# Performance work log

Hardware: AMD Instinct MI355X
Metric: run time of the kernel (lower is better)

The kernel has to match this reference:

```python
import jax, jax.numpy as jnp
import numpy as np

B, D_IN, D_FEAT, N_EX, N_LAB = 4096, 512, 512, 20000, 100
P_FACTOR = 3.0
EPS = 1e-12  # torch F.normalize eps


def setup_inputs() -> dict:
    key = jax.random.key(0)
    k1, k2, k3, k4 = jax.random.split(key, 4)
    features = jax.random.normal(k1, (B, D_IN), dtype=jnp.float32)
    g_weight = jax.random.normal(k2, (D_FEAT, D_IN), dtype=jnp.float32) * (1.0 / np.sqrt(D_IN))
    ex_features = jax.random.normal(k3, (N_EX, D_IN), dtype=jnp.float32)
    ex_classes = jax.random.uniform(k4, (N_EX, N_LAB), dtype=jnp.float32)
    class_reps = jnp.eye(N_LAB, dtype=jnp.float32)  # one_hot(arange(num_labels)) since class_dim is None
    return {"features": features, "g_weight": g_weight, "ex_features": ex_features,
            "ex_classes": ex_classes, "class_reps": class_reps}


def _l2_normalize(x):
    n = jnp.linalg.norm(x, axis=-1, keepdims=True)
    return x / jnp.maximum(n, EPS)


def _l1_normalize(x):
    n = jnp.sum(jnp.abs(x), axis=-1, keepdims=True)
    return x / jnp.maximum(n, EPS)


def reference(features, g_weight, ex_features, ex_classes, class_reps):
    # g projection (bias-free linear)
    f = features @ g_weight.T          # [B, D_FEAT]
    e = ex_features @ g_weight.T       # [N_EX, D_FEAT]
    # exemplar class representations
    ex_class_reps = _l1_normalize(ex_classes) @ class_reps  # [N_EX, N_LAB]
    # cosine similarity
    s = _l2_normalize(f) @ _l2_normalize(e).T  # [B, N_EX]
    # power-sign activation then L1 row-normalize
    a = jnp.sign(s) * jnp.abs(s) ** P_FACTOR
    a = _l1_normalize(a)
    echo = a @ ex_class_reps           # [B, N_LAB]
    return echo
```

## Files before the change

kernel.cpp:

```cpp
#include <hip/hip_runtime.h>

#define B_ROWS 4096
#define D      512
#define N_EX   20000
#define EXP2   20096
#define MPROJ  24192
#define N_LAB  100
#define LABP2  128
#define NT2    157
#define SPLITS 16

typedef __attribute__((ext_vector_type(8)))  short short8v;
typedef __attribute__((ext_vector_type(16))) float f32x16;
typedef __attribute__((ext_vector_type(2)))  int   int2v;
typedef unsigned short u16;

__device__ __forceinline__ u16 f2bf(float x) {
    unsigned u = __builtin_bit_cast(unsigned, x);
    u = u + 0x7FFFu + ((u >> 16) & 1u);
    return (u16)(u >> 16);
}
__device__ __forceinline__ float bf2f(u16 h) {
    unsigned u = ((unsigned)h) << 16;
    return __builtin_bit_cast(float, u);
}

__device__ __forceinline__ void gload16(const void* g, void* l) {
    __builtin_amdgcn_global_load_lds((const __attribute__((address_space(1))) void*)g,
                                     (__attribute__((address_space(3))) void*)l, 16, 0, 0);
}

__device__ __forceinline__ unsigned pk_bf16(float a, float b) {
    unsigned r;
    asm("v_cvt_pk_bf16_f32 %0, %1, %2" : "=v"(r) : "v"(a), "v"(b));
    return r;
}

__device__ __forceinline__ void swap_halves(unsigned &a, unsigned &b) {
#if __has_builtin(__builtin_amdgcn_permlane32_swap)
    int2v r = __builtin_amdgcn_permlane32_swap((int)a, (int)b, false, false);
    a = (unsigned)r[0]; b = (unsigned)r[1];
#else
    unsigned sa = (unsigned)__shfl_xor((int)a, 32, 64);
    unsigned sb = (unsigned)__shfl_xor((int)b, 32, 64);
    if (threadIdx.x & 32) a = sb; else b = sa;
#endif
}

#define MFMA32(a, b, c) __builtin_amdgcn_mfma_f32_32x32x16_bf16((a), (b), (c), 0, 0, 0)

__global__ __launch_bounds__(256)
void split3_k(const float* __restrict__ f, const float* __restrict__ ex,
              const float* __restrict__ gw, u16* __restrict__ xall,
              u16* __restrict__ wh) {
    int i8 = blockIdx.x * 256 + threadIdx.x;
    int row = i8 >> 6;
    int e = (i8 & 63) * 8;
    const float* src = nullptr;
    u16* dst;
    if (row < B_ROWS) {
        src = &f[(size_t)row * D + e];
        dst = &xall[(size_t)row * D + e];
    } else if (row < B_ROWS + EXP2) {
        int er = row - B_ROWS;
        if (er < N_EX) src = &ex[(size_t)er * D + e];
        dst = &xall[(size_t)row * D + e];
    } else if (row < B_ROWS + EXP2 + D) {
        int wr = row - B_ROWS - EXP2;
        src = &gw[(size_t)wr * D + e];
        dst = &wh[(size_t)wr * D + e];
    } else return;
    short8v h = {0,0,0,0,0,0,0,0};
    if (src) {
        float4 a = *(const float4*)src, b = *(const float4*)(src + 4);
        float v[8] = {a.x,a.y,a.z,a.w,b.x,b.y,b.z,b.w};
        #pragma unroll
        for (int j = 0; j < 8; ++j) h[j] = (short)f2bf(v[j]);
    }
    *(short8v*)dst = h;
}

__global__ __launch_bounds__(512, 4)
void gemm128_k(const u16* __restrict__ A, const u16* __restrict__ B,
               u16* __restrict__ C) {
    __shared__ u16 BUF[2][128][128];
    const int tid = threadIdx.x;
    const int l = tid & 63, w = tid >> 6;
    const int wa = w >> 2, wb = w & 3;
    const int l31 = l & 31, l5 = l >> 5;
    const int m0 = blockIdx.x * 128, n0 = blockIdx.y * 128;
    const int qrow_in = l >> 4;
    const int gs = l & 15;

    f32x16 sacc[2] = {};

    auto STAGE = [&](int nx, int kc_) {
        const int kofs = kc_ * 64;
        #pragma unroll
        for (int i = 0; i < 4; ++i) {
            const int q = w * 4 + i;
            const int r = q * 4 + qrow_in;
            const int g = gs ^ (r & 15);
            const u16* src = (g < 8)
                ? &A[(size_t)(m0 + r) * D + kofs + g * 8]
                : &B[(size_t)(n0 + r) * D + kofs + (g - 8) * 8];
            gload16(src, (u16*)&BUF[nx][0][0] + q * 512);
        }
    };

    STAGE(0, 0);
    __syncthreads();
    int cur = 0;
    for (int kc = 0; kc < 8; ++kc) {
        if (kc < 7) STAGE(cur ^ 1, kc + 1);
        const u16* base = &BUF[cur][0][0];
        #pragma unroll
        for (int ks = 0; ks < 4; ++ks) {
            const int gk = ks * 2 + l5;
            short8v aX[2], bW;
            #pragma unroll
            for (int ei = 0; ei < 2; ++ei) {
                int r = wa * 64 + ei * 32 + l31;
                aX[ei] = *(const short8v*)(base + r * 128 + (gk ^ (r & 15)) * 8);
            }
            {
                int r = wb * 32 + l31;
                bW = *(const short8v*)(base + r * 128 + ((gk | 8) ^ (r & 15)) * 8);
            }
            sacc[0] = MFMA32(aX[0], bW, sacc[0]);
            sacc[1] = MFMA32(aX[1], bW, sacc[1]);
        }
        __syncthreads();
        cur ^= 1;
    }
    #pragma unroll
    for (int ei = 0; ei < 2; ++ei)
        #pragma unroll
        for (int r = 0; r < 16; ++r) {
            int row = m0 + wa * 64 + ei * 32 + (r & 3) + 8 * (r >> 2) + 4 * l5;
            int col = n0 + wb * 32 + l31;
            C[(size_t)row * D + col] = f2bf(sacc[ei][r]);
        }
}

__global__ __launch_bounds__(256)
void l2norm_k(u16* __restrict__ hi, int nrows) {
    const int row = blockIdx.x * 4 + (threadIdx.x >> 6);
    const int ln = threadIdx.x & 63;
    if (row >= nrows) return;
    const size_t base = (size_t)row * D + ln * 8;
    short8v hv = *(short8v*)&hi[base];
    float v[8]; float ss = 0.f;
    #pragma unroll
    for (int j = 0; j < 8; ++j) { v[j] = bf2f((u16)hv[j]); ss += v[j] * v[j]; }
    #pragma unroll
    for (int off = 32; off > 0; off >>= 1) ss += __shfl_xor(ss, off, 64);
    float inv = 1.0f / fmaxf(sqrtf(ss), 1e-12f);
    short8v ho;
    #pragma unroll
    for (int j = 0; j < 8; ++j) ho[j] = (short)f2bf(v[j] * inv);
    *(short8v*)&hi[base] = ho;
}

__global__ __launch_bounds__(256)
void ecrT_k(const float* __restrict__ exc, const float* __restrict__ creps,
            u16* __restrict__ th) {
    __shared__ float CRT[N_LAB][101];
    __shared__ float EX[128][N_LAB];
    __shared__ float INV[128];
    __shared__ u16 OUT[LABP2][128];
    const int tid = threadIdx.x;
    const int e0 = blockIdx.x * 128;
    for (int i = tid; i < N_LAB * N_LAB; i += 256) {
        int c = i / N_LAB, lab = i % N_LAB;
        CRT[lab][c] = creps[i];
    }
    for (int i = tid; i < 128 * N_LAB; i += 256) {
        int el = i / N_LAB, c = i % N_LAB;
        int e = e0 + el;
        EX[el][c] = (e < N_EX) ? exc[(size_t)e * N_LAB + c] : 0.f;
    }
    __syncthreads();
    if (tid < 128) {
        float s = 0.f;
        for (int c = 0; c < N_LAB; ++c) s += fabsf(EX[tid][c]);
        INV[tid] = 1.0f / fmaxf(s, 1e-12f);
    }
    __syncthreads();
    const int lab = tid & 127;
    for (int el = tid >> 7; el < 128; el += 2) {
        float acc = 0.f;
        if (lab < N_LAB) {
            #pragma unroll 4
            for (int c = 0; c < N_LAB; ++c) acc += EX[el][c] * CRT[lab][c];
            acc *= INV[el];
        }
        OUT[lab][el] = f2bf(acc);
    }
    __syncthreads();
    for (int i = tid; i < LABP2 * 16; i += 256) {
        int lb = i >> 4, ch = i & 15;
        *(short8v*)&th[(size_t)lb * EXP2 + e0 + ch * 8] = *(const short8v*)&OUT[lb][ch * 8];
    }
}

__global__ __launch_bounds__(512, 2)
void fused_k(const u16* __restrict__ fnh, const u16* __restrict__ enh,
             const u16* __restrict__ ecth,
             float* __restrict__ nump, float* __restrict__ denp2) {
    __shared__ u16 SMEM[65536];
    u16* ENR = SMEM;
    u16* FNR = SMEM + 16384;
    u16* WTB = SMEM + 49152;

    const int tid = threadIdx.x;
    const int l = tid & 63, w = tid >> 6;
    const int we = w >> 2, wq = w & 3;
    const int l31 = l & 31, l5 = l >> 5;
    const int m0 = blockIdx.x * 256;
    const int split = blockIdx.y;

    union FragU { short8v s; unsigned u[4]; };

    f32x16 num_acc[2][4] = {};
    float den_th[2] = {0.f, 0.f};

    auto STAGE_AB = [&](int nx, int t_, int kc_) {
        const int e0_ = t_ * 128, kofs = kc_ * 64;
        #pragma unroll
        for (int i = 0; i < 2; ++i) {
            const int p = w * 128 + i * 64 + l;
            const int line = p >> 4, q = (p & 15) ^ (line & 15);
            const int row = line * 2 + (q >> 3), g = q & 7;
            gload16(&enh[(size_t)(e0_ + row) * D + kofs + g * 8],
                    ENR + nx * 8192 + p * 8);
        }
        #pragma unroll
        for (int i = 0; i < 4; ++i) {
            const int p = w * 256 + i * 64 + l;
            const int line = p >> 4, q = (p & 15) ^ (line & 15);
            const int row = line * 2 + (q >> 3), g = q & 7;
            gload16(&fnh[(size_t)(m0 + row) * D + kofs + g * 8],
                    FNR + nx * 16384 + p * 8);
        }
    };
    auto STAGE_WT = [&](int t_) {
        const int e0_ = t_ * 128;
        #pragma unroll
        for (int i = 0; i < 4; ++i) {
            const int p = w * 256 + i * 64 + l;
            const int lab = p >> 4, g = p & 15;
            gload16(&ecth[(size_t)lab * EXP2 + e0_ + ((g ^ (lab & 15)) * 8)],
                    WTB + p * 8);
        }
    };
    auto ldfrag = [&](const u16* base, int r, int gk) -> short8v {
        int line = r >> 1;
        int slot = (((r & 1) << 3) | gk) ^ (line & 15);
        return *(const short8v*)(base + line * 128 + slot * 8);
    };

    STAGE_AB(0, split, 0);
    int cur = 0;

    for (int t = split; t < NT2; t += SPLITS) {
        f32x16 sacc[2][2] = {};
        for (int kc = 0; kc < 8; ++kc) {
            if (kc < 7) {
                STAGE_AB(cur ^ 1, t, kc + 1);
                asm volatile("s_waitcnt vmcnt(6)" ::: "memory");
            } else {
                STAGE_WT(t);
                asm volatile("s_waitcnt vmcnt(4)" ::: "memory");
            }
            __builtin_amdgcn_s_barrier();
            __builtin_amdgcn_sched_barrier(0);
            const u16* eb = ENR + cur * 8192;
            const u16* fb = FNR + cur * 16384;
            __builtin_amdgcn_s_setprio(1);
            #pragma unroll
            for (int ks = 0; ks < 4; ++ks) {
                const int gk = ks * 2 + l5;
                short8v aE[2], bF[2];
                #pragma unroll
                for (int ei = 0; ei < 2; ++ei)
                    aE[ei] = ldfrag(eb, we * 64 + ei * 32 + l31, gk);
                #pragma unroll
                for (int mi = 0; mi < 2; ++mi)
                    bF[mi] = ldfrag(fb, wq * 64 + mi * 32 + l31, gk);
                #pragma unroll
                for (int ei = 0; ei < 2; ++ei)
                    #pragma unroll
                    for (int mi = 0; mi < 2; ++mi)
                        sacc[ei][mi] = MFMA32(aE[ei], bF[mi], sacc[ei][mi]);
            }
            __builtin_amdgcn_s_setprio(0);
            asm volatile("s_waitcnt lgkmcnt(0)" ::: "memory");
            __builtin_amdgcn_sched_barrier(0);
            __builtin_amdgcn_s_barrier();
            if (kc < 7) cur ^= 1;
        }
        const int tn = t + SPLITS;
        if (tn < NT2) {
            STAGE_AB(cur ^ 1, tn, 0);
            asm volatile("s_waitcnt vmcnt(6)" ::: "memory");
        } else {
            asm volatile("s_waitcnt vmcnt(0)" ::: "memory");
        }
        __builtin_amdgcn_s_barrier();
        __builtin_amdgcn_sched_barrier(0);
        #pragma unroll
        for (int ei = 0; ei < 2; ++ei) {
            FragU fr[2][2];
            #pragma unroll
            for (int mi = 0; mi < 2; ++mi) {
                float a3[16];
                #pragma unroll
                for (int r = 0; r < 16; ++r) {
                    float sv = sacc[ei][mi][r];
                    float c3 = sv * sv * sv;
                    a3[r] = c3;
                    den_th[mi] += fabsf(c3);
                }
                #pragma unroll
                for (int c = 0; c < 2; ++c) {
                    unsigned p01 = pk_bf16(a3[c*8+0], a3[c*8+1]);
                    unsigned p23 = pk_bf16(a3[c*8+2], a3[c*8+3]);
                    unsigned p45 = pk_bf16(a3[c*8+4], a3[c*8+5]);
                    unsigned p67 = pk_bf16(a3[c*8+6], a3[c*8+7]);
                    swap_halves(p01, p45);
                    swap_halves(p23, p67);
                    fr[mi][c].u[0] = p01; fr[mi][c].u[1] = p23;
                    fr[mi][c].u[2] = p45; fr[mi][c].u[3] = p67;
                }
            }
            __builtin_amdgcn_s_setprio(1);
            #pragma unroll
            for (int c = 0; c < 2; ++c) {
                const int gw = (we * 4 + ei * 2 + c) * 2 + l5;
                #pragma unroll
                for (int lt = 0; lt < 4; ++lt) {
                    int row = lt * 32 + l31;
                    short8v wf = *(const short8v*)(WTB + row * 128 + (gw ^ (row & 15)) * 8);
                    num_acc[0][lt] = MFMA32(fr[0][c].s, wf, num_acc[0][lt]);
                    num_acc[1][lt] = MFMA32(fr[1][c].s, wf, num_acc[1][lt]);
                }
            }
            __builtin_amdgcn_s_setprio(0);
        }
        asm volatile("s_waitcnt lgkmcnt(0)" ::: "memory");
        __builtin_amdgcn_sched_barrier(0);
        __builtin_amdgcn_s_barrier();
        cur ^= 1;
    }

    #pragma unroll
    for (int mi = 0; mi < 2; ++mi) {
        float v = den_th[mi];
        v += __shfl_xor(v, 32, 64);
        if (l5 == 0)
            denp2[((size_t)split * 2 + we) * B_ROWS + m0 + wq * 64 + mi * 32 + l31] = v;
    }

    float* SMf = (float*)SMEM;
    __syncthreads();
    #pragma unroll
    for (int half = 0; half < 2; ++half) {
        if (we == 1 && (wq >> 1) == half) {
            #pragma unroll
            for (int mi = 0; mi < 2; ++mi)
                #pragma unroll
                for (int lt = 0; lt < 4; ++lt)
                    #pragma unroll
                    for (int r = 0; r < 16; ++r) {
                        int rowf = (r & 3) + 8 * (r >> 2) + 4 * l5;
                        int lrow = (wq & 1) * 64 + mi * 32 + rowf;
                        SMf[lrow * 128 + lt * 32 + l31] = num_acc[mi][lt][r];
                    }
        }
        __syncthreads();
        if (we == 0 && (wq >> 1) == half) {
            #pragma unroll
            for (int mi = 0; mi < 2; ++mi)
                #pragma unroll
                for (int lt = 0; lt < 4; ++lt)
                    #pragma unroll
                    for (int r = 0; r < 16; ++r) {
                        int rowf = (r & 3) + 8 * (r >> 2) + 4 * l5;
                        int lrow = (wq & 1) * 64 + mi * 32 + rowf;
                        float v = num_acc[mi][lt][r] + SMf[lrow * 128 + lt * 32 + l31];
                        int m = m0 + wq * 64 + mi * 32 + rowf;
                        nump[((size_t)split * B_ROWS + m) * LABP2 + lt * 32 + l31] = v;
                    }
        }
        __syncthreads();
    }
}

__global__ __launch_bounds__(128)
void finalize_k(const float* __restrict__ nump, const float* __restrict__ denp2,
                float* __restrict__ out) {
    const int row = blockIdx.x, tid = threadIdx.x;
    float den = 0.f;
    for (int s = 0; s < 2 * SPLITS; ++s)
        den += denp2[(size_t)s * B_ROWS + row];
    if (tid < N_LAB) {
        float acc = 0.f;
        for (int s = 0; s < SPLITS; ++s)
            acc += nump[((size_t)s * B_ROWS + row) * LABP2 + tid];
        out[(size_t)row * N_LAB + tid] = acc / fmaxf(den, 1e-12f);
    }
}

extern "C" void kernel_launch(void* const* d_in, const int* in_sizes, int n_in,
                              void* d_out, int out_size, void* d_ws, size_t ws_size,
                              hipStream_t stream) {
    (void)in_sizes; (void)n_in; (void)out_size; (void)ws_size;
    const float* features    = (const float*)d_in[0];
    const float* g_weight    = (const float*)d_in[1];
    const float* ex_features = (const float*)d_in[2];
    const float* ex_classes  = (const float*)d_in[3];
    const float* class_reps  = (const float*)d_in[4];
    float* out = (float*)d_out;

    size_t off = 0;
    auto alloc = [&](size_t bytes) {
        void* p = (char*)d_ws + off;
        off += (bytes + 255) & ~(size_t)255;
        return p;
    };
    u16* fnh = (u16*)alloc((size_t)B_ROWS * D * 2);
    u16* enh = (u16*)alloc((size_t)EXP2 * D * 2);
    u16* ecth = (u16*)alloc((size_t)LABP2 * EXP2 * 2);
    u16* wh  = (u16*)alloc((size_t)D * D * 2);
    float* nump  = (float*)alloc((size_t)SPLITS * B_ROWS * LABP2 * 4);
    float* denp2 = (float*)alloc((size_t)2 * SPLITS * B_ROWS * 4);
    u16* xall = (u16*)nump;

    const int tot_rows = B_ROWS + EXP2 + D;
    split3_k<<<(tot_rows * 64 + 255) / 256, 256, 0, stream>>>(
        features, ex_features, g_weight, xall, wh);
    gemm128_k<<<dim3(MPROJ / 128, 4), 512, 0, stream>>>(xall, wh, fnh);
    l2norm_k<<<(MPROJ + 3) / 4, 256, 0, stream>>>(fnh, MPROJ);
    ecrT_k<<<NT2, 256, 0, stream>>>(ex_classes, class_reps, ecth);
    fused_k<<<dim3(B_ROWS / 256, SPLITS), 512, 0, stream>>>(fnh, enh, ecth, nump, denp2);
    finalize_k<<<B_ROWS, 128, 0, stream>>>(nump, denp2, out);
}
```

Measured before the change: 400.7 us.

## Remap fused kernel grid per XCD and simplify pipeline synchronization

Flattens the fused kernel grid to 1D and assigns splits from the block index so each XCD handles only two split values across all row tiles. Blocks on one XCD then reuse the same exemplar and weight tiles from that XCD's L2 instead of fetching them separately. It also replaces the hand-tuned vmcnt waits, raw s_barrier/sched_barrier and setprio hints with plain __syncthreads, adding one after the initial prefetch. That keeps the double-buffered prefetch overlapping the MFMA work but waits more conservatively, and may lose some scheduling control.

```diff
diff --git a/kernel.cpp b/kernel.cpp
--- a/kernel.cpp
+++ b/kernel.cpp
@@ -217,8 +217,9 @@
     const int l = tid & 63, w = tid >> 6;
     const int we = w >> 2, wq = w & 3;
     const int l31 = l & 31, l5 = l >> 5;
-    const int m0 = blockIdx.x * 256;
-    const int split = blockIdx.y;
+    const int wg = blockIdx.x;
+    const int split = (wg & 7) + 8 * ((wg >> 3) & 1);
+    const int m0 = (wg >> 4) * 256;
 
     union FragU { short8v s; unsigned u[4]; };
 
@@ -261,23 +262,16 @@
     };
 
     STAGE_AB(0, split, 0);
+    __syncthreads();
     int cur = 0;
 
     for (int t = split; t < NT2; t += SPLITS) {
         f32x16 sacc[2][2] = {};
         for (int kc = 0; kc < 8; ++kc) {
-            if (kc < 7) {
-                STAGE_AB(cur ^ 1, t, kc + 1);
-                asm volatile("s_waitcnt vmcnt(6)" ::: "memory");
-            } else {
-                STAGE_WT(t);
-                asm volatile("s_waitcnt vmcnt(4)" ::: "memory");
-            }
-            __builtin_amdgcn_s_barrier();
-            __builtin_amdgcn_sched_barrier(0);
+            if (kc < 7) STAGE_AB(cur ^ 1, t, kc + 1);
+            else        STAGE_WT(t);
             const u16* eb = ENR + cur * 8192;
             const u16* fb = FNR + cur * 16384;
-            __builtin_amdgcn_s_setprio(1);
             #pragma unroll
             for (int ks = 0; ks < 4; ++ks) {
                 const int gk = ks * 2 + l5;
@@ -294,21 +288,11 @@
                     for (int mi = 0; mi < 2; ++mi)
                         sacc[ei][mi] = MFMA32(aE[ei], bF[mi], sacc[ei][mi]);
             }
-            __builtin_amdgcn_s_setprio(0);
-            asm volatile("s_waitcnt lgkmcnt(0)" ::: "memory");
-            __builtin_amdgcn_sched_barrier(0);
-            __builtin_amdgcn_s_barrier();
+            __syncthreads();
             if (kc < 7) cur ^= 1;
         }
         const int tn = t + SPLITS;
-        if (tn < NT2) {
-            STAGE_AB(cur ^ 1, tn, 0);
-            asm volatile("s_waitcnt vmcnt(6)" ::: "memory");
-        } else {
-            asm volatile("s_waitcnt vmcnt(0)" ::: "memory");
-        }
-        __builtin_amdgcn_s_barrier();
-        __builtin_amdgcn_sched_barrier(0);
+        if (tn < NT2) STAGE_AB(cur ^ 1, tn, 0);
         #pragma unroll
         for (int ei = 0; ei < 2; ++ei) {
             FragU fr[2][2];
@@ -334,23 +318,19 @@
                     fr[mi][c].u[2] = p45; fr[mi][c].u[3] = p67;
                 }
             }
-            __builtin_amdgcn_s_setprio(1);
             #pragma unroll
             for (int c = 0; c < 2; ++c) {
-                const int gw = (we * 4 + ei * 2 + c) * 2 + l5;
+                const int gw2 = (we * 4 + ei * 2 + c) * 2 + l5;
                 #pragma unroll
                 for (int lt = 0; lt < 4; ++lt) {
                     int row = lt * 32 + l31;
-                    short8v wf = *(const short8v*)(WTB + row * 128 + (gw ^ (row & 15)) * 8);
+                    short8v wf = *(const short8v*)(WTB + row * 128 + (gw2 ^ (row & 15)) * 8);
                     num_acc[0][lt] = MFMA32(fr[0][c].s, wf, num_acc[0][lt]);
                     num_acc[1][lt] = MFMA32(fr[1][c].s, wf, num_acc[1][lt]);
                 }
             }
-            __builtin_amdgcn_s_setprio(0);
-        }
-        asm volatile("s_waitcnt lgkmcnt(0)" ::: "memory");
-        __builtin_amdgcn_sched_barrier(0);
-        __builtin_amdgcn_s_barrier();
+        }
+        __syncthreads();
         cur ^= 1;
     }
 
@@ -443,6 +423,6 @@
     gemm128_k<<<dim3(MPROJ / 128, 4), 512, 0, stream>>>(xall, wh, fnh);
     l2norm_k<<<(MPROJ + 3) / 4, 256, 0, stream>>>(fnh, MPROJ);
     ecrT_k<<<NT2, 256, 0, stream>>>(ex_classes, class_reps, ecth);
-    fused_k<<<dim3(B_ROWS / 256, SPLITS), 512, 0, stream>>>(fnh, enh, ecth, nump, denp2);
+    fused_k<<<256, 512, 0, stream>>>(fnh, enh, ecth, nump, denp2);
     finalize_k<<<B_ROWS, 128, 0, stream>>>(nump, denp2, out);
 }
```

Result: faster. 376.2 us (median of 3 runs) (-6.1%).

## Drop in-place L2 normalization; fold exemplar inverse-norm cubed into activation

Applied to the files above, without the earlier changes.

Replaces the in-place L2 normalize pass over all projected rows with a kernel that stores only each exemplar row's inverse norm cubed. That factor is then multiplied into the cubed similarity inside the fused kernel. The feature-row normalization is skipped because the later L1 row-normalization cancels a per-row scale. The change also flattens the fused grid to 1D with a remapped split/row order and removes the sched_barrier/setprio hints. In exchange it adds 16 scattered global loads per fragment in the epilogue, and bf16 range and precision now depend on the unnormalized magnitudes.

```diff
diff --git a/kernel.cpp b/kernel.cpp
--- a/kernel.cpp
+++ b/kernel.cpp
@@ -144,22 +144,20 @@
 }
 
 __global__ __launch_bounds__(256)
-void l2norm_k(u16* __restrict__ hi, int nrows) {
+void inve3_k(const u16* __restrict__ enh, float* __restrict__ inve3) {
     const int row = blockIdx.x * 4 + (threadIdx.x >> 6);
     const int ln = threadIdx.x & 63;
-    if (row >= nrows) return;
-    const size_t base = (size_t)row * D + ln * 8;
-    short8v hv = *(short8v*)&hi[base];
-    float v[8]; float ss = 0.f;
+    if (row >= EXP2) return;
+    short8v hv = *(const short8v*)&enh[(size_t)row * D + ln * 8];
+    float ss = 0.f;
     #pragma unroll
-    for (int j = 0; j < 8; ++j) { v[j] = bf2f((u16)hv[j]); ss += v[j] * v[j]; }
+    for (int j = 0; j < 8; ++j) { float v = bf2f((u16)hv[j]); ss += v * v; }
     #pragma unroll
     for (int off = 32; off > 0; off >>= 1) ss += __shfl_xor(ss, off, 64);
-    float inv = 1.0f / fmaxf(sqrtf(ss), 1e-12f);
-    short8v ho;
-    #pragma unroll
-    for (int j = 0; j < 8; ++j) ho[j] = (short)f2bf(v[j] * inv);
-    *(short8v*)&hi[base] = ho;
+    if (ln == 0) {
+        float q = (ss > 0.f) ? rsqrtf(ss) : 0.f;
+        inve3[row] = q * q * q;
+    }
 }
 
 __global__ __launch_bounds__(256)
@@ -206,7 +204,7 @@
 
 __global__ __launch_bounds__(512, 2)
 void fused_k(const u16* __restrict__ fnh, const u16* __restrict__ enh,
-             const u16* __restrict__ ecth,
+             const u16* __restrict__ ecth, const float* __restrict__ inve3,
              float* __restrict__ nump, float* __restrict__ denp2) {
     __shared__ u16 SMEM[65536];
     u16* ENR = SMEM;
@@ -217,8 +215,9 @@
     const int l = tid & 63, w = tid >> 6;
     const int we = w >> 2, wq = w & 3;
     const int l31 = l & 31, l5 = l >> 5;
-    const int m0 = blockIdx.x * 256;
-    const int split = blockIdx.y;
+    const int wg = blockIdx.x;
+    const int split = (wg & 7) + 8 * ((wg >> 3) & 1);
+    const int m0 = (wg >> 4) * 256;
 
     union FragU { short8v s; unsigned u[4]; };
 
@@ -264,6 +263,7 @@
     int cur = 0;
 
     for (int t = split; t < NT2; t += SPLITS) {
+        const int e0 = t * 128;
         f32x16 sacc[2][2] = {};
         for (int kc = 0; kc < 8; ++kc) {
             if (kc < 7) {
@@ -274,10 +274,8 @@
                 asm volatile("s_waitcnt vmcnt(4)" ::: "memory");
             }
             __builtin_amdgcn_s_barrier();
-            __builtin_amdgcn_sched_barrier(0);
             const u16* eb = ENR + cur * 8192;
             const u16* fb = FNR + cur * 16384;
-            __builtin_amdgcn_s_setprio(1);
             #pragma unroll
             for (int ks = 0; ks < 4; ++ks) {
                 const int gk = ks * 2 + l5;
@@ -294,9 +292,7 @@
                     for (int mi = 0; mi < 2; ++mi)
                         sacc[ei][mi] = MFMA32(aE[ei], bF[mi], sacc[ei][mi]);
             }
-            __builtin_amdgcn_s_setprio(0);
             asm volatile("s_waitcnt lgkmcnt(0)" ::: "memory");
-            __builtin_amdgcn_sched_barrier(0);
             __builtin_amdgcn_s_barrier();
             if (kc < 7) cur ^= 1;
         }
@@ -308,9 +304,12 @@
             asm volatile("s_waitcnt vmcnt(0)" ::: "memory");
         }
         __builtin_amdgcn_s_barrier();
-        __builtin_amdgcn_sched_barrier(0);
         #pragma unroll
         for (int ei = 0; ei < 2; ++ei) {
+            float iv[16];
+            #pragma unroll
+            for (int r = 0; r < 16; ++r)
+                iv[r] = inve3[e0 + we * 64 + ei * 32 + (r & 3) + 8 * (r >> 2) + 4 * l5];
             FragU fr[2][2];
             #pragma unroll
             for (int mi = 0; mi < 2; ++mi) {
@@ -318,7 +317,7 @@
                 #pragma unroll
                 for (int r = 0; r < 16; ++r) {
                     float sv = sacc[ei][mi][r];
-                    float c3 = sv * sv * sv;
+                    float c3 = sv * sv * sv * iv[r];
                     a3[r] = c3;
                     den_th[mi] += fabsf(c3);
                 }
@@ -334,22 +333,19 @@
                     fr[mi][c].u[2] = p45; fr[mi][c].u[3] = p67;
                 }
             }
-            __builtin_amdgcn_s_setprio(1);
             #pragma unroll
             for (int c = 0; c < 2; ++c) {
-                const int gw = (we * 4 + ei * 2 + c) * 2 + l5;
+                const int gw2 = (we * 4 + ei * 2 + c) * 2 + l5;
                 #pragma unroll
                 for (int lt = 0; lt < 4; ++lt) {
                     int row = lt * 32 + l31;
-                    short8v wf = *(const short8v*)(WTB + row * 128 + (gw ^ (row & 15)) * 8);
+                    short8v wf = *(const short8v*)(WTB + row * 128 + (gw2 ^ (row & 15)) * 8);
                     num_acc[0][lt] = MFMA32(fr[0][c].s, wf, num_acc[0][lt]);
                     num_acc[1][lt] = MFMA32(fr[1][c].s, wf, num_acc[1][lt]);
                 }
             }
-            __builtin_amdgcn_s_setprio(0);
         }
         asm volatile("s_waitcnt lgkmcnt(0)" ::: "memory");
-        __builtin_amdgcn_sched_barrier(0);
         __builtin_amdgcn_s_barrier();
         cur ^= 1;
     }
@@ -433,6 +429,7 @@
     u16* enh = (u16*)alloc((size_t)EXP2 * D * 2);
     u16* ecth = (u16*)alloc((size_t)LABP2 * EXP2 * 2);
     u16* wh  = (u16*)alloc((size_t)D * D * 2);
+    float* inve3 = (float*)alloc((size_t)EXP2 * 4);
     float* nump  = (float*)alloc((size_t)SPLITS * B_ROWS * LABP2 * 4);
     float* denp2 = (float*)alloc((size_t)2 * SPLITS * B_ROWS * 4);
     u16* xall = (u16*)nump;
@@ -441,8 +438,8 @@
     split3_k<<<(tot_rows * 64 + 255) / 256, 256, 0, stream>>>(
         features, ex_features, g_weight, xall, wh);
     gemm128_k<<<dim3(MPROJ / 128, 4), 512, 0, stream>>>(xall, wh, fnh);
-    l2norm_k<<<(MPROJ + 3) / 4, 256, 0, stream>>>(fnh, MPROJ);
+    inve3_k<<<(EXP2 + 3) / 4, 256, 0, stream>>>(enh, inve3);
     ecrT_k<<<NT2, 256, 0, stream>>>(ex_classes, class_reps, ecth);
-    fused_k<<<dim3(B_ROWS / 256, SPLITS), 512, 0, stream>>>(fnh, enh, ecth, nump, denp2);
+    fused_k<<<256, 512, 0, stream>>>(fnh, enh, ecth, inve3, nump, denp2);
     finalize_k<<<B_ROWS, 128, 0, stream>>>(nump, denp2, out);
 }
```

After: 391.2 us. 1.02x faster.
